# Kernel tuning notes

Measured on AMD Instinct MI355X. Metric: run time of the kernel, lower is better.

## Reference

```python
import jax, jax.numpy as jnp
import numpy as np

K = 16  # nsample


def _conv2d(x, w, b=None):
    # 1x1 conv2d: x [B,Cin,K,N], w [Cout,Cin]
    y = jnp.einsum('oc,bckn->bokn', w, x)
    return y if b is None else y + b[None, :, None, None]


def setup_inputs() -> dict:
    key = jax.random.key(0)
    ks = jax.random.split(key, 20)
    B, N1, N2, C = 2, 4096, 8192, 64
    Cin = C + 3  # in_channel + 3
    w = lambda k, shape, fan: (jax.random.normal(k, shape, jnp.float32) / np.sqrt(fan).astype(np.float32))
    return {
        'xyz1': jax.random.normal(ks[0], (B, 3, N1), jnp.float32),
        'xyz2': jax.random.normal(ks[1], (B, 3, N2), jnp.float32),
        'points1': jax.random.normal(ks[2], (B, C, N1), jnp.float32),
        'points2': jax.random.normal(ks[3], (B, C, N2), jnp.float32),
        'w_r0': w(ks[4], (C, Cin), Cin), 'b_r0': jnp.zeros((C,), jnp.float32),
        'w_r1': w(ks[5], (C, C), C), 'b_r1': jnp.zeros((C,), jnp.float32),
        'w_z0': w(ks[6], (C, Cin), Cin), 'b_z0': jnp.zeros((C,), jnp.float32),
        'w_z1': w(ks[7], (C, C), C), 'b_z1': jnp.zeros((C,), jnp.float32),
        'w_h0': w(ks[8], (C, Cin), Cin), 'b_h0': jnp.zeros((C,), jnp.float32),
        'w_h1': w(ks[9], (C, C), C), 'b_h1': jnp.zeros((C,), jnp.float32),
        'w_fuse_r': w(ks[10], (C, C), C),
        'w_fuse_z': w(ks[11], (C, C), C),
        'w_fuse_ro': w(ks[12], (C, C), C),
    }


def reference(xyz1, xyz2, points1, points2,
              w_r0, b_r0, w_r1, b_r1,
              w_z0, b_z0, w_z1, b_z1,
              w_h0, b_h0, w_h1, b_h1,
              w_fuse_r, w_fuse_z, w_fuse_ro):
    x1 = jnp.transpose(xyz1, (0, 2, 1))  # [B,N1,3]
    x2 = jnp.transpose(xyz2, (0, 2, 1))  # [B,N2,3]
    # squared pairwise distances [B,N1,N2]
    sq = (jnp.sum(x1 * x1, -1)[:, :, None]
          + jnp.sum(x2 * x2, -1)[:, None, :]
          - 2.0 * jnp.einsum('bnd,bmd->bnm', x1, x2))
    _, knn = jax.lax.top_k(-sq, K)  # [B,N1,K] smallest distances
    gather = jax.vmap(lambda p, i: p[i])
    nbr_xyz = gather(x2, knn)                 # [B,N1,K,3]
    dir_xyz = nbr_xyz - x1[:, :, None, :]
    p2 = gather(jnp.transpose(points2, (0, 2, 1)), knn)  # [B,N1,K,C]
    new_pts = jnp.transpose(jnp.concatenate([p2, dir_xyz], -1), (0, 3, 2, 1))  # [B,C+3,K,N1]

    lrelu = lambda v: jax.nn.leaky_relu(v, 0.1)
    fuse = lambda w, p: jnp.einsum('oc,bcn->bon', w, p)

    # r gate
    r = _conv2d(new_pts, w_r0, b_r0) + fuse(w_fuse_r, points1)[:, :, None, :]
    r = lrelu(r)
    r = jax.nn.sigmoid(_conv2d(r, w_r1, b_r1))  # [B,C,K,N1]

    # z gate (max over neighbors before last conv)
    z = _conv2d(new_pts, w_z0, b_z0) + fuse(w_fuse_z, points1)[:, :, None, :]
    z = lrelu(z)
    z = jnp.max(z, axis=2, keepdims=True)
    z = jax.nn.sigmoid(_conv2d(z, w_z1, b_z1))[:, :, 0, :]  # [B,C,N1]

    # h candidate
    p1e = _conv2d(r * points1[:, :, None, :], w_fuse_ro)
    h = lrelu(_conv2d(new_pts, w_h0, b_h0) + p1e)
    h = jnp.max(h, axis=2, keepdims=True)
    h = jnp.tanh(_conv2d(h, w_h1, b_h1))[:, :, 0, :]  # [B,C,N1]

    return (1.0 - z) * points1 + z * h
```

## Files before the change

### kernel.cpp

```cpp
#include <hip/hip_runtime.h>
#include <math.h>

typedef __attribute__((ext_vector_type(8))) short bf8_t;
typedef __attribute__((ext_vector_type(4))) float f32x4;

#define NB   2
#define N1S  4096
#define N2S  8192
#define CC   64
#define KK   16
#define GQ   8

#define M_R0 0
#define M_Z0 1
#define M_H0 2
#define M_R1 3
#define M_Z1 4
#define M_H1 5
#define M_FR 6
#define M_FZ 7
#define M_FRO 8

#define WA_SHORTS   (9*4*2*64*8)
#define WDIR_OFF    (WA_SHORTS*2)
#define WDIR_FLOATS (3*3*64)
#define XP_OFF      (WDIR_OFF + WDIR_FLOATS*4)
#define XP_BYTES    (NB*N2S*16)
#define KIDX_OFF    (XP_OFF + XP_BYTES)
#define KIDX_BYTES  (NB*N1S*KK*4)
#define P2T_OFF     (KIDX_OFF + KIDX_BYTES)
#define P2T_BYTES   ((size_t)NB*N2S*CC*4)

__device__ __forceinline__ float lrelu(float v){ return v > 0.f ? v : 0.1f*v; }
__device__ __forceinline__ float sigm(float v){ return 1.f/(1.f + __expf(-v)); }
__device__ __forceinline__ float tanh_(float v){ return 1.f - 2.f/(__expf(2.f*v) + 1.f); }
__device__ __forceinline__ unsigned short f2bf(float f){
  union { float f; unsigned u; } v; v.f = f;
  unsigned r = v.u + 0x7FFF + ((v.u >> 16) & 1);
  return (unsigned short)(r >> 16);
}

__global__ __launch_bounds__(256) void prep_wA(
    const float* __restrict__ r0, const float* __restrict__ z0, const float* __restrict__ h0,
    const float* __restrict__ r1, const float* __restrict__ z1, const float* __restrict__ h1,
    const float* __restrict__ fr, const float* __restrict__ fz, const float* __restrict__ fro,
    short* __restrict__ wa, float* __restrict__ wdir)
{
  const float* W[9] = {r0, z0, h0, r1, z1, h1, fr, fz, fro};
  const int Ks[9]   = {67, 67, 67, 64, 64, 64, 64, 64, 64};
  const int stride = gridDim.x * 256;
  for (int i = blockIdx.x*256 + threadIdx.x; i < WA_SHORTS; i += stride) {
    const int j = i & 7, l = (i >> 3) & 63, kk = (i >> 9) & 1, r = (i >> 10) & 3, mat = i >> 12;
    const int row = r*16 + (l & 15);
    const int c = kk*32 + ((l >> 4) << 3) + j;
    wa[i] = (short)f2bf(W[mat][row*Ks[mat] + c]);
  }
  for (int i = blockIdx.x*256 + threadIdx.x; i < WDIR_FLOATS; i += stride) {
    const int g = i / 192, rem = i % 192, d = rem / 64, o = rem & 63;
    wdir[i] = W[g][o*67 + 64 + d];
  }
}

__global__ __launch_bounds__(256) void pack_xyz2(const float* __restrict__ xyz2, float4* __restrict__ xp){
  const int i = blockIdx.x*256 + threadIdx.x;
  const int b = i >> 13, j = i & (N2S-1);
  const float x = xyz2[((size_t)(b*3+0))*N2S + j];
  const float y = xyz2[((size_t)(b*3+1))*N2S + j];
  const float z = xyz2[((size_t)(b*3+2))*N2S + j];
  xp[i] = make_float4(x, y, z, (x*x + y*y) + z*z);
}

__global__ __launch_bounds__(256) void transpose_p2(const float* __restrict__ src, float* __restrict__ dst){
  __shared__ float t[64][65];
  const int b = blockIdx.y; const int j0 = blockIdx.x*64;
  const int tx = threadIdx.x & 63; const int r4 = threadIdx.x >> 6;
  #pragma unroll
  for (int c = r4; c < 64; c += 4) t[c][tx] = src[((size_t)b*CC + c)*N2S + j0 + tx];
  __syncthreads();
  #pragma unroll
  for (int j = r4; j < 64; j += 4) dst[((size_t)b*N2S + j0 + j)*CC + tx] = t[tx][j];
}

__global__ __launch_bounds__(256) void knn_kernel(
    const float* __restrict__ xyz1, const float4* __restrict__ xp, int* __restrict__ idxout)
{
  const int tid = threadIdx.x, w = tid >> 6, lane = tid & 63, grp = lane >> 4;
  const int qbase = blockIdx.x*8 + w*2;
  const int b = qbase >> 12;
  const float4* __restrict__ X = xp + (b << 13);
  float qx[2], qy[2], qz[2], s1[2], kth[2];
  #pragma unroll
  for (int g = 0; g < 2; g++) {
    const int n = (qbase + g) & (N1S-1);
    qx[g] = xyz1[((size_t)(b*3+0))*N1S + n];
    qy[g] = xyz1[((size_t)(b*3+1))*N1S + n];
    qz[g] = xyz1[((size_t)(b*3+2))*N1S + n];
    s1[g] = (qx[g]*qx[g] + qy[g]*qy[g]) + qz[g]*qz[g];
    kth[g] = INFINITY;
  }
  float listd = INFINITY; int listi = 0;
  for (int c0 = 0; c0 < N2S; c0 += 128) {
    const float4 v0 = X[c0 + lane];
    const float4 v1 = X[c0 + 64 + lane];
    #pragma unroll
    for (int h = 0; h < 2; h++) {
      const float4 v = h ? v1 : v0;
      const int base = c0 + h*64;
      #pragma unroll
      for (int g = 0; g < 2; g++) {
        const float d = (s1[g] + v.w) - 2.f*((qx[g]*v.x + qy[g]*v.y) + qz[g]*v.z);
        unsigned long long vote = __ballot(d < kth[g]);
        while (vote) {
          const int src = (int)__builtin_ctzll(vote);
          vote &= vote - 1;
          const float dv = __shfl(d, src);
          if (dv < kth[g]) {
            const int iv = base + src;
            const float ud = __shfl_up(listd, 1);
            const int   ui = __shfl_up(listi, 1);
            const bool ing = (grp == g);
            const bool cm = ing && (dv < listd);
            const bool cp = cm && ((lane & 15) > 0) && (dv < ud);
            listd = cm ? (cp ? ud : dv) : listd;
            listi = cm ? (cp ? ui : iv) : listi;
            kth[g] = __shfl(listd, g*16 + 15);
          }
        }
      }
    }
  }
  if (grp < 2) idxout[(size_t)(qbase + grp)*KK + (lane & 15)] = listi;
}

#define FRAG(mat, kk) (*(const bf8_t*)(wA + (((mat)*4 + w)*2 + (kk))*512 + lane*8))

__global__ __launch_bounds__(256) void gates_kernel(
    const float* __restrict__ xyz1, const float* __restrict__ xyz2,
    const float* __restrict__ points1, const float* __restrict__ p2t,
    const int* __restrict__ kidx, const short* __restrict__ wA,
    const float* __restrict__ wdir,
    const float* __restrict__ b_r0, const float* __restrict__ b_z0,
    const float* __restrict__ b_h0, const float* __restrict__ b_r1,
    const float* __restrict__ b_z1, const float* __restrict__ b_h1,
    float* __restrict__ out)
{
  __shared__ __align__(16) short featB[2][GQ][64][8];
  __shared__ __align__(16) short rB[2][GQ][64][8];
  __shared__ __align__(16) float p1f[64][GQ];
  __shared__ __align__(16) short p1B[2][64][8];
  __shared__ float BFr[64][GQ], BFz[64][GQ];
  __shared__ float zmaxL[64][GQ], hmaxL[64][GQ];
  __shared__ float biasL[6][64];
  __shared__ float dirL[3][GQ*KK];
  __shared__ __align__(16) float obuf[64][GQ];

  const int tid = threadIdx.x;
  const int w = tid >> 6, lane = tid & 63;
  const int b  = blockIdx.x >> 9;
  const int n0 = (blockIdx.x & 511) * GQ;
  const int cq = lane & 15;
  const int reg_o0 = w*16 + ((lane >> 4) << 2);
  const f32x4 zero4 = {0.f, 0.f, 0.f, 0.f};

  for (int i = tid; i < 6*64; i += 256) {
    const int a = i >> 6, o = i & 63;
    const float* bp = (a==0)?b_r0:(a==1)?b_z0:(a==2)?b_h0:(a==3)?b_r1:(a==4)?b_z1:b_h1;
    biasL[a][o] = bp[o];
  }
  if (tid < 64) {
    const float* sp = points1 + ((size_t)(b*CC + tid))*N1S + n0;
    *(float4*)&p1f[tid][0] = ((const float4*)sp)[0];
    *(float4*)&p1f[tid][4] = ((const float4*)sp)[1];
  }
  ((unsigned long long*)&p1B[0][0][0])[tid] = 0ULL;
  if (tid < 128) {
    const int m = tid, qg = n0 + (m >> 4);
    const int j = kidx[(size_t)((b << 12) + qg)*KK + (m & 15)];
    #pragma unroll
    for (int d = 0; d < 3; d++)
      dirL[d][m] = xyz2[((size_t)(b*3+d))*N2S + j] - xyz1[((size_t)(b*3+d))*N1S + qg];
  }
  {
    const int m = tid >> 1, half = tid & 1;
    const int qg = n0 + (m >> 4);
    const int j = kidx[(size_t)((b << 12) + qg)*KK + (m & 15)];
    const float* __restrict__ src = p2t + ((size_t)(b << 13) + j)*CC + half*32;
    float v[32];
    #pragma unroll
    for (int i = 0; i < 8; i++) {
      const float4 f = ((const float4*)src)[i];
      v[i*4] = f.x; v[i*4+1] = f.y; v[i*4+2] = f.z; v[i*4+3] = f.w;
    }
    #pragma unroll
    for (int gi = 0; gi < 4; gi++) {
      bf8_t pk;
      #pragma unroll
      for (int j2 = 0; j2 < 8; j2++) pk[j2] = (short)f2bf(v[gi*8 + j2]);
      *(bf8_t*)&featB[half][m >> 4][gi*16 + (m & 15)][0] = pk;
    }
  }
  __syncthreads();

  {
    const int s0 = tid*4;
    const int j0 = s0 & 7, l = (s0 >> 3) & 63, kk = s0 >> 9;
    const int q = l & 15;
    if (q < 8) {
      unsigned short t0[4];
      #pragma unroll
      for (int jj = 0; jj < 4; jj++)
        t0[jj] = f2bf(p1f[kk*32 + ((l >> 4) << 3) + j0 + jj][q]);
      uint2 pk; pk.x = t0[0] | ((unsigned)t0[1] << 16); pk.y = t0[2] | ((unsigned)t0[3] << 16);
      *(uint2*)&p1B[kk][l][j0] = pk;
    }
  }
  __syncthreads();

  {
    const bf8_t fa0 = FRAG(M_FR, 0), fa1 = FRAG(M_FR, 1);
    const bf8_t ga0 = FRAG(M_FZ, 0), ga1 = FRAG(M_FZ, 1);
    const bf8_t pb0 = *(const bf8_t*)&p1B[0][lane][0];
    const bf8_t pb1 = *(const bf8_t*)&p1B[1][lane][0];
    f32x4 ar = __builtin_amdgcn_mfma_f32_16x16x32_bf16(fa0, pb0, zero4, 0, 0, 0);
    ar = __builtin_amdgcn_mfma_f32_16x16x32_bf16(fa1, pb1, ar, 0, 0, 0);
    f32x4 az = __builtin_amdgcn_mfma_f32_16x16x32_bf16(ga0, pb0, zero4, 0, 0, 0);
    az = __builtin_amdgcn_mfma_f32_16x16x32_bf16(ga1, pb1, az, 0, 0, 0);
    if (cq < 8) {
      #pragma unroll
      for (int r2 = 0; r2 < 4; r2++) {
        const int o = reg_o0 + r2;
        BFr[o][cq] = ar[r2] + biasL[0][o];
        BFz[o][cq] = az[r2] + biasL[1][o];
      }
    }
  }

  {
    const bf8_t ra0 = FRAG(M_R0, 0), ra1 = FRAG(M_R0, 1);
    const bf8_t za0 = FRAG(M_Z0, 0), za1 = FRAG(M_Z0, 1);
    float wdr[3][4], wdz[3][4];
    #pragma unroll
    for (int d = 0; d < 3; d++)
      #pragma unroll
      for (int r2 = 0; r2 < 4; r2++) {
        wdr[d][r2] = wdir[(0*3 + d)*64 + reg_o0 + r2];
        wdz[d][r2] = wdir[(1*3 + d)*64 + reg_o0 + r2];
      }
    const int kkv = reg_o0 >> 5, lp = ((reg_o0 & 31) >> 3)*16 + cq, j0 = reg_o0 & 7;
    #pragma unroll
    for (int ct = 0; ct < GQ; ct++) {
      const bf8_t fb0 = *(const bf8_t*)&featB[0][ct][lane][0];
      const bf8_t fb1 = *(const bf8_t*)&featB[1][ct][lane][0];
      f32x4 accr = __builtin_amdgcn_mfma_f32_16x16x32_bf16(ra0, fb0, zero4, 0, 0, 0);
      accr = __builtin_amdgcn_mfma_f32_16x16x32_bf16(ra1, fb1, accr, 0, 0, 0);
      f32x4 accz = __builtin_amdgcn_mfma_f32_16x16x32_bf16(za0, fb0, zero4, 0, 0, 0);
      accz = __builtin_amdgcn_mfma_f32_16x16x32_bf16(za1, fb1, accz, 0, 0, 0);
      const int m = ct*16 + cq;
      const float d0 = dirL[0][m], d1 = dirL[1][m], d2 = dirL[2][m];
      unsigned short rpk[4]; float zv[4];
      #pragma unroll
      for (int r2 = 0; r2 < 4; r2++) {
        const int o = reg_o0 + r2;
        float rv = accr[r2] + BFr[o][ct] + wdr[0][r2]*d0 + wdr[1][r2]*d1 + wdr[2][r2]*d2;
        rpk[r2] = f2bf(lrelu(rv));
        float zt = accz[r2] + BFz[o][ct] + wdz[0][r2]*d0 + wdz[1][r2]*d1 + wdz[2][r2]*d2;
        zv[r2] = lrelu(zt);
      }
      uint2 pk; pk.x = rpk[0] | ((unsigned)rpk[1] << 16); pk.y = rpk[2] | ((unsigned)rpk[3] << 16);
      *(uint2*)&rB[kkv][ct][lp][j0] = pk;
      #pragma unroll
      for (int r2 = 0; r2 < 4; r2++) {
        float vv = zv[r2];
        vv = fmaxf(vv, __shfl_xor(vv, 1));
        vv = fmaxf(vv, __shfl_xor(vv, 2));
        vv = fmaxf(vv, __shfl_xor(vv, 4));
        vv = fmaxf(vv, __shfl_xor(vv, 8));
        zv[r2] = vv;
      }
      if (cq == 0) {
        #pragma unroll
        for (int r2 = 0; r2 < 4; r2++) zmaxL[reg_o0 + r2][ct] = zv[r2];
      }
    }
  }
  __syncthreads();

  uint2 rpK[GQ];
  float zg[4];
  {
    const bf8_t r1a0 = FRAG(M_R1, 0), r1a1 = FRAG(M_R1, 1);
    #pragma unroll
    for (int ct = 0; ct < GQ; ct++) {
      const bf8_t b0 = *(const bf8_t*)&rB[0][ct][lane][0];
      const bf8_t b1 = *(const bf8_t*)&rB[1][ct][lane][0];
      f32x4 acc = __builtin_amdgcn_mfma_f32_16x16x32_bf16(r1a0, b0, zero4, 0, 0, 0);
      acc = __builtin_amdgcn_mfma_f32_16x16x32_bf16(r1a1, b1, acc, 0, 0, 0);
      unsigned short pk4[4];
      #pragma unroll
      for (int r2 = 0; r2 < 4; r2++) {
        const int o = reg_o0 + r2;
        const float rg = sigm(acc[r2] + biasL[3][o]);
        pk4[r2] = f2bf(rg * p1f[o][ct]);
      }
      rpK[ct].x = pk4[0] | ((unsigned)pk4[1] << 16);
      rpK[ct].y = pk4[2] | ((unsigned)pk4[3] << 16);
    }
    const bf8_t z1a0 = FRAG(M_Z1, 0), z1a1 = FRAG(M_Z1, 1);
    const int qc = cq < 8 ? cq : 7;
    bf8_t zb0, zb1;
    #pragma unroll
    for (int j = 0; j < 8; j++) {
      zb0[j] = (short)f2bf(zmaxL[((lane >> 4) << 3) + j][qc]);
      zb1[j] = (short)f2bf(zmaxL[32 + ((lane >> 4) << 3) + j][qc]);
    }
    f32x4 az = __builtin_amdgcn_mfma_f32_16x16x32_bf16(z1a0, zb0, zero4, 0, 0, 0);
    az = __builtin_amdgcn_mfma_f32_16x16x32_bf16(z1a1, zb1, az, 0, 0, 0);
    #pragma unroll
    for (int r2 = 0; r2 < 4; r2++) zg[r2] = sigm(az[r2] + biasL[4][reg_o0 + r2]);
  }
  __syncthreads();

  {
    const int kkv = reg_o0 >> 5, lp = ((reg_o0 & 31) >> 3)*16 + cq, j0 = reg_o0 & 7;
    #pragma unroll
    for (int ct = 0; ct < GQ; ct++) *(uint2*)&rB[kkv][ct][lp][j0] = rpK[ct];
  }
  __syncthreads();

  {
    const bf8_t h0a0 = FRAG(M_H0, 0), h0a1 = FRAG(M_H0, 1);
    const bf8_t foa0 = FRAG(M_FRO, 0), foa1 = FRAG(M_FRO, 1);
    float wdh[3][4];
    #pragma unroll
    for (int d = 0; d < 3; d++)
      #pragma unroll
      for (int r2 = 0; r2 < 4; r2++) wdh[d][r2] = wdir[(2*3 + d)*64 + reg_o0 + r2];
    #pragma unroll
    for (int ct = 0; ct < GQ; ct++) {
      const bf8_t fb0 = *(const bf8_t*)&featB[0][ct][lane][0];
      const bf8_t fb1 = *(const bf8_t*)&featB[1][ct][lane][0];
      const bf8_t rb0 = *(const bf8_t*)&rB[0][ct][lane][0];
      const bf8_t rb1 = *(const bf8_t*)&rB[1][ct][lane][0];
      f32x4 acc = __builtin_amdgcn_mfma_f32_16x16x32_bf16(h0a0, fb0, zero4, 0, 0, 0);
      acc = __builtin_amdgcn_mfma_f32_16x16x32_bf16(h0a1, fb1, acc, 0, 0, 0);
      acc = __builtin_amdgcn_mfma_f32_16x16x32_bf16(foa0, rb0, acc, 0, 0, 0);
      acc = __builtin_amdgcn_mfma_f32_16x16x32_bf16(foa1, rb1, acc, 0, 0, 0);
      const int m = ct*16 + cq;
      const float d0 = dirL[0][m], d1 = dirL[1][m], d2 = dirL[2][m];
      float hv[4];
      #pragma unroll
      for (int r2 = 0; r2 < 4; r2++) {
        const int o = reg_o0 + r2;
        hv[r2] = lrelu(acc[r2] + biasL[2][o] + wdh[0][r2]*d0 + wdh[1][r2]*d1 + wdh[2][r2]*d2);
      }
      #pragma unroll
      for (int r2 = 0; r2 < 4; r2++) {
        float vv = hv[r2];
        vv = fmaxf(vv, __shfl_xor(vv, 1));
        vv = fmaxf(vv, __shfl_xor(vv, 2));
        vv = fmaxf(vv, __shfl_xor(vv, 4));
        vv = fmaxf(vv, __shfl_xor(vv, 8));
        hv[r2] = vv;
      }
      if (cq == 0) {
        #pragma unroll
        for (int r2 = 0; r2 < 4; r2++) hmaxL[reg_o0 + r2][ct] = hv[r2];
      }
    }
  }
  __syncthreads();

  {
    const bf8_t h1a0 = FRAG(M_H1, 0), h1a1 = FRAG(M_H1, 1);
    const int qc = cq < 8 ? cq : 7;
    bf8_t hb0, hb1;
    #pragma unroll
    for (int j = 0; j < 8; j++) {
      hb0[j] = (short)f2bf(hmaxL[((lane >> 4) << 3) + j][qc]);
      hb1[j] = (short)f2bf(hmaxL[32 + ((lane >> 4) << 3) + j][qc]);
    }
    f32x4 ah = __builtin_amdgcn_mfma_f32_16x16x32_bf16(h1a0, hb0, zero4, 0, 0, 0);
    ah = __builtin_amdgcn_mfma_f32_16x16x32_bf16(h1a1, hb1, ah, 0, 0, 0);
    if (cq < 8) {
      #pragma unroll
      for (int r2 = 0; r2 < 4; r2++) {
        const int o = reg_o0 + r2;
        const float hg = tanh_(ah[r2] + biasL[5][o]);
        obuf[o][cq] = (1.f - zg[r2])*p1f[o][cq] + zg[r2]*hg;
      }
    }
  }
  __syncthreads();
  if (tid < 128) {
    const int c = tid >> 1, q4 = (tid & 1)*4;
    *(float4*)(out + ((size_t)(b*CC + c))*N1S + n0 + q4) = *(float4*)&obuf[c][q4];
  }
}

extern "C" void kernel_launch(void* const* d_in, const int* in_sizes, int n_in,
                              void* d_out, int out_size, void* d_ws, size_t ws_size,
                              hipStream_t stream) {
  const float* xyz1    = (const float*)d_in[0];
  const float* xyz2    = (const float*)d_in[1];
  const float* points1 = (const float*)d_in[2];
  const float* points2 = (const float*)d_in[3];
  const float* w_r0 = (const float*)d_in[4];
  const float* b_r0 = (const float*)d_in[5];
  const float* w_r1 = (const float*)d_in[6];
  const float* b_r1 = (const float*)d_in[7];
  const float* w_z0 = (const float*)d_in[8];
  const float* b_z0 = (const float*)d_in[9];
  const float* w_z1 = (const float*)d_in[10];
  const float* b_z1 = (const float*)d_in[11];
  const float* w_h0 = (const float*)d_in[12];
  const float* b_h0 = (const float*)d_in[13];
  const float* w_h1 = (const float*)d_in[14];
  const float* b_h1 = (const float*)d_in[15];
  const float* w_fr  = (const float*)d_in[16];
  const float* w_fz  = (const float*)d_in[17];
  const float* w_fro = (const float*)d_in[18];
  float* out = (float*)d_out;

  short*  wa   = (short*)d_ws;
  float*  wdir = (float*)((char*)d_ws + WDIR_OFF);
  float4* xp   = (float4*)((char*)d_ws + XP_OFF);
  int*    kidx = (int*)((char*)d_ws + KIDX_OFF);
  float*  p2t  = (float*)((char*)d_ws + P2T_OFF);

  prep_wA<<<16, 256, 0, stream>>>(w_r0, w_z0, w_h0, w_r1, w_z1, w_h1,
                                  w_fr, w_fz, w_fro, wa, wdir);
  pack_xyz2<<<64, 256, 0, stream>>>(xyz2, xp);
  transpose_p2<<<dim3(N2S/64, NB), dim3(256), 0, stream>>>(points2, p2t);

  knn_kernel<<<1024, 256, 0, stream>>>(xyz1, xp, kidx);

  gates_kernel<<<1024, 256, 0, stream>>>(
      xyz1, xyz2, points1, p2t, kidx, wa, wdir,
      b_r0, b_z0, b_h0, b_r1, b_z1, b_h1, out);
}
```

Before: 211.2 us.

## Prefilter KNN with per-lane minima threshold, LDS tiling, and bf16 points2 staging

The KNN kernel now makes a first pass over LDS-staged tiles of xyz2 that tracks each lane's minimum distance per query. A bitonic sort across the wave turns those 64 minima into a threshold (kappa) that bounds the 16th-nearest distance, which prunes insertions in the second pass. Each wave now handles 4 queries and the grid is halved. A fallback rescans from scratch for any query whose list did not fill. Separately, points2 is converted to bf16 during the transpose, so the gates kernel gathers half the bytes and no longer converts per element. The extra pass adds distance compute and a second LDS streaming sweep.

```diff
diff --git a/kernel.cpp b/kernel.cpp
--- a/kernel.cpp
+++ b/kernel.cpp
@@ -10,6 +10,7 @@
 #define CC   64
 #define KK   16
 #define GQ   8
+#define KTILE 2048
 
 #define M_R0 0
 #define M_Z0 1
@@ -28,8 +29,8 @@
 #define XP_BYTES    (NB*N2S*16)
 #define KIDX_OFF    (XP_OFF + XP_BYTES)
 #define KIDX_BYTES  (NB*N1S*KK*4)
-#define P2T_OFF     (KIDX_OFF + KIDX_BYTES)
-#define P2T_BYTES   ((size_t)NB*N2S*CC*4)
+#define P2B_OFF     (KIDX_OFF + KIDX_BYTES)
+#define P2B_BYTES   ((size_t)NB*N2S*CC*2)
 
 __device__ __forceinline__ float lrelu(float v){ return v > 0.f ? v : 0.1f*v; }
 __device__ __forceinline__ float sigm(float v){ return 1.f/(1.f + __expf(-v)); }
@@ -70,7 +71,7 @@
   xp[i] = make_float4(x, y, z, (x*x + y*y) + z*z);
 }
 
-__global__ __launch_bounds__(256) void transpose_p2(const float* __restrict__ src, float* __restrict__ dst){
+__global__ __launch_bounds__(256) void transpose_p2(const float* __restrict__ src, unsigned short* __restrict__ dst){
   __shared__ float t[64][65];
   const int b = blockIdx.y; const int j0 = blockIdx.x*64;
   const int tx = threadIdx.x & 63; const int r4 = threadIdx.x >> 6;
@@ -78,44 +79,74 @@
   for (int c = r4; c < 64; c += 4) t[c][tx] = src[((size_t)b*CC + c)*N2S + j0 + tx];
   __syncthreads();
   #pragma unroll
-  for (int j = r4; j < 64; j += 4) dst[((size_t)b*N2S + j0 + j)*CC + tx] = t[tx][j];
+  for (int j = r4; j < 64; j += 4) dst[((size_t)b*N2S + j0 + j)*CC + tx] = f2bf(t[tx][j]);
 }
 
 __global__ __launch_bounds__(256) void knn_kernel(
     const float* __restrict__ xyz1, const float4* __restrict__ xp, int* __restrict__ idxout)
 {
+  __shared__ float4 T[KTILE];
   const int tid = threadIdx.x, w = tid >> 6, lane = tid & 63, grp = lane >> 4;
-  const int qbase = blockIdx.x*8 + w*2;
+  const int qbase = blockIdx.x*16 + w*4;
   const int b = qbase >> 12;
   const float4* __restrict__ X = xp + (b << 13);
-  float qx[2], qy[2], qz[2], s1[2], kth[2];
+  float qx[4], qy[4], qz[4], s1[4], kth[4], kappa[4], m[4];
   #pragma unroll
-  for (int g = 0; g < 2; g++) {
+  for (int g = 0; g < 4; g++) {
     const int n = (qbase + g) & (N1S-1);
     qx[g] = xyz1[((size_t)(b*3+0))*N1S + n];
     qy[g] = xyz1[((size_t)(b*3+1))*N1S + n];
     qz[g] = xyz1[((size_t)(b*3+2))*N1S + n];
     s1[g] = (qx[g]*qx[g] + qy[g]*qy[g]) + qz[g]*qz[g];
-    kth[g] = INFINITY;
-  }
+    kth[g] = INFINITY; m[g] = INFINITY;
+  }
+
+  for (int t0 = 0; t0 < N2S; t0 += KTILE) {
+    __syncthreads();
+    for (int i = tid; i < KTILE; i += 256) T[i] = X[t0 + i];
+    __syncthreads();
+    for (int c0 = 0; c0 < KTILE; c0 += 64) {
+      const float4 v = T[c0 + lane];
+      #pragma unroll
+      for (int g = 0; g < 4; g++) {
+        const float d = (s1[g] + v.w) - 2.f*((qx[g]*v.x + qy[g]*v.y) + qz[g]*v.z);
+        m[g] = fminf(m[g], d);
+      }
+    }
+  }
+  #pragma unroll
+  for (int g = 0; g < 4; g++) {
+    float v = m[g];
+    #pragma unroll
+    for (int k = 2; k <= 64; k <<= 1) {
+      #pragma unroll
+      for (int j = k >> 1; j > 0; j >>= 1) {
+        const float pv = __shfl_xor(v, j);
+        const bool up = ((lane & k) == 0);
+        const bool keepmin = up ? ((lane & j) == 0) : ((lane & j) != 0);
+        v = keepmin ? fminf(v, pv) : fmaxf(v, pv);
+      }
+    }
+    kappa[g] = __shfl(v, 16);
+  }
+
   float listd = INFINITY; int listi = 0;
-  for (int c0 = 0; c0 < N2S; c0 += 128) {
-    const float4 v0 = X[c0 + lane];
-    const float4 v1 = X[c0 + 64 + lane];
-    #pragma unroll
-    for (int h = 0; h < 2; h++) {
-      const float4 v = h ? v1 : v0;
-      const int base = c0 + h*64;
-      #pragma unroll
-      for (int g = 0; g < 2; g++) {
+  for (int t0 = 0; t0 < N2S; t0 += KTILE) {
+    __syncthreads();
+    for (int i = tid; i < KTILE; i += 256) T[i] = X[t0 + i];
+    __syncthreads();
+    for (int c0 = 0; c0 < KTILE; c0 += 64) {
+      const float4 v = T[c0 + lane];
+      #pragma unroll
+      for (int g = 0; g < 4; g++) {
         const float d = (s1[g] + v.w) - 2.f*((qx[g]*v.x + qy[g]*v.y) + qz[g]*v.z);
-        unsigned long long vote = __ballot(d < kth[g]);
+        unsigned long long vote = __ballot(d < fminf(kth[g], kappa[g]));
         while (vote) {
           const int src = (int)__builtin_ctzll(vote);
           vote &= vote - 1;
           const float dv = __shfl(d, src);
           if (dv < kth[g]) {
-            const int iv = base + src;
+            const int iv = t0 + c0 + src;
             const float ud = __shfl_up(listd, 1);
             const int   ui = __shfl_up(listi, 1);
             const bool ing = (grp == g);
@@ -129,14 +160,50 @@
       }
     }
   }
-  if (grp < 2) idxout[(size_t)(qbase + grp)*KK + (lane & 15)] = listi;
+
+  {
+    bool need = false;
+    #pragma unroll
+    for (int g = 0; g < 4; g++) need = need || (kth[g] == INFINITY);
+    if (__builtin_expect(need, 0)) {
+      #pragma unroll
+      for (int g = 0; g < 4; g++) {
+        if (kth[g] == INFINITY) {
+          if (grp == g) { listd = INFINITY; listi = 0; }
+          float kk2 = INFINITY;
+          for (int c0 = 0; c0 < N2S; c0 += 64) {
+            const float4 v = X[c0 + lane];
+            const float d = (s1[g] + v.w) - 2.f*((qx[g]*v.x + qy[g]*v.y) + qz[g]*v.z);
+            unsigned long long vote = __ballot(d < kk2);
+            while (vote) {
+              const int src = (int)__builtin_ctzll(vote);
+              vote &= vote - 1;
+              const float dv = __shfl(d, src);
+              if (dv < kk2) {
+                const int iv = c0 + src;
+                const float ud = __shfl_up(listd, 1);
+                const int   ui = __shfl_up(listi, 1);
+                const bool ing = (grp == g);
+                const bool cm = ing && (dv < listd);
+                const bool cp = cm && ((lane & 15) > 0) && (dv < ud);
+                listd = cm ? (cp ? ud : dv) : listd;
+                listi = cm ? (cp ? ui : iv) : listi;
+                kk2 = __shfl(listd, g*16 + 15);
+              }
+            }
+          }
+        }
+      }
+    }
+  }
+  idxout[(size_t)(qbase + grp)*KK + (lane & 15)] = listi;
 }
 
 #define FRAG(mat, kk) (*(const bf8_t*)(wA + (((mat)*4 + w)*2 + (kk))*512 + lane*8))
 
 __global__ __launch_bounds__(256) void gates_kernel(
     const float* __restrict__ xyz1, const float* __restrict__ xyz2,
-    const float* __restrict__ points1, const float* __restrict__ p2t,
+    const float* __restrict__ points1, const unsigned short* __restrict__ p2b,
     const int* __restrict__ kidx, const short* __restrict__ wA,
     const float* __restrict__ wdir,
     const float* __restrict__ b_r0, const float* __restrict__ b_z0,
@@ -182,22 +249,13 @@
   }
   {
     const int m = tid >> 1, half = tid & 1;
-    const int qg = n0 + (m >> 4);
+    const int ct = m >> 4;
+    const int qg = n0 + ct;
     const int j = kidx[(size_t)((b << 12) + qg)*KK + (m & 15)];
-    const float* __restrict__ src = p2t + ((size_t)(b << 13) + j)*CC + half*32;
-    float v[32];
-    #pragma unroll
-    for (int i = 0; i < 8; i++) {
-      const float4 f = ((const float4*)src)[i];
-      v[i*4] = f.x; v[i*4+1] = f.y; v[i*4+2] = f.z; v[i*4+3] = f.w;
-    }
-    #pragma unroll
-    for (int gi = 0; gi < 4; gi++) {
-      bf8_t pk;
-      #pragma unroll
-      for (int j2 = 0; j2 < 8; j2++) pk[j2] = (short)f2bf(v[gi*8 + j2]);
-      *(bf8_t*)&featB[half][m >> 4][gi*16 + (m & 15)][0] = pk;
-    }
+    const uint4* __restrict__ src = (const uint4*)(p2b + (((size_t)(b << 13) + j)*CC + half*32));
+    #pragma unroll
+    for (int gi = 0; gi < 4; gi++)
+      *(uint4*)&featB[half][ct][gi*16 + (m & 15)][0] = src[gi];
   }
   __syncthreads();
 
@@ -425,16 +483,16 @@
   float*  wdir = (float*)((char*)d_ws + WDIR_OFF);
   float4* xp   = (float4*)((char*)d_ws + XP_OFF);
   int*    kidx = (int*)((char*)d_ws + KIDX_OFF);
-  float*  p2t  = (float*)((char*)d_ws + P2T_OFF);
+  unsigned short* p2b = (unsigned short*)((char*)d_ws + P2B_OFF);
 
   prep_wA<<<16, 256, 0, stream>>>(w_r0, w_z0, w_h0, w_r1, w_z1, w_h1,
                                   w_fr, w_fz, w_fro, wa, wdir);
   pack_xyz2<<<64, 256, 0, stream>>>(xyz2, xp);
-  transpose_p2<<<dim3(N2S/64, NB), dim3(256), 0, stream>>>(points2, p2t);
-
-  knn_kernel<<<1024, 256, 0, stream>>>(xyz1, xp, kidx);
+  transpose_p2<<<dim3(N2S/64, NB), dim3(256), 0, stream>>>(points2, p2b);
+
+  knn_kernel<<<512, 256, 0, stream>>>(xyz1, xp, kidx);
 
   gates_kernel<<<1024, 256, 0, stream>>>(
-      xyz1, xyz2, points1, p2t, kidx, wa, wdir,
+      xyz1, xyz2, points1, p2b, kidx, wa, wdir,
       b_r0, b_z0, b_h0, b_r1, b_z1, b_h1, out);
 }
```

Measured after the change: 198.8 us. -5.8%, faster.
